# Kernel tuning notes

Measured on AMD Instinct MI355X. Metric: run time of the kernel, lower is better.

The kernel has to match this reference:

```python
import jax, jax.numpy as jnp
import numpy as np

N = 100000      # nodes
E = 1600000     # edges (before self loops)
F_IN = 128      # num_features
HEADS1, CH1 = 8, 8    # conv1: heads=8, out=8, concat -> 64
HEADS2, CH2 = 1, 16   # conv2: heads=1, out=16, concat=False
B = 64          # graphs in batch


def setup_inputs() -> dict:
    key = jax.random.key(0)
    ks = jax.random.split(key, 20)
    s = 0.05
    x = jax.random.normal(ks[0], (N, F_IN), dtype=jnp.float32)
    edge_index = jax.random.randint(ks[1], (2, E), 0, N, dtype=jnp.int64)
    batch = jnp.sort(jax.random.randint(ks[2], (N,), 0, B, dtype=jnp.int64))
    d = {
        'x': x, 'edge_index': edge_index, 'batch': batch,
        # conv1 params (GATv2: lin_l / lin_r with bias, att vector, output bias)
        'Wl1': jax.random.normal(ks[3], (F_IN, HEADS1 * CH1)) * s,
        'bl1': jnp.zeros((HEADS1 * CH1,), jnp.float32),
        'Wr1': jax.random.normal(ks[4], (F_IN, HEADS1 * CH1)) * s,
        'br1': jnp.zeros((HEADS1 * CH1,), jnp.float32),
        'att1': jax.random.normal(ks[5], (HEADS1, CH1)) * s,
        'bias1': jnp.zeros((HEADS1 * CH1,), jnp.float32),
        # conv2 params
        'Wl2': jax.random.normal(ks[6], (HEADS1 * CH1, HEADS2 * CH2)) * s,
        'bl2': jnp.zeros((HEADS2 * CH2,), jnp.float32),
        'Wr2': jax.random.normal(ks[7], (HEADS1 * CH1, HEADS2 * CH2)) * s,
        'br2': jnp.zeros((HEADS2 * CH2,), jnp.float32),
        'att2': jax.random.normal(ks[8], (HEADS2, CH2)) * s,
        'bias2': jnp.zeros((CH2,), jnp.float32),
        # classifier 16 -> 1
        'Wc': jax.random.normal(ks[9], (CH2, 1)) * s,
        'bc': jnp.zeros((1,), jnp.float32),
    }
    return d


def gatv2_layer(x, src, dst, Wl, bl, Wr, br, att, bias, heads, ch, concat):
    n = x.shape[0]
    xl = (x @ Wl + bl).reshape(n, heads, ch)   # source transform (messages)
    xr = (x @ Wr + br).reshape(n, heads, ch)   # target transform
    m = xl[src] + xr[dst]                      # [E, H, C]
    e = jax.nn.leaky_relu(m, 0.2)
    logits = jnp.einsum('ehc,hc->eh', e, att)  # [E, H]
    # segment softmax over incoming edges per target node
    mx = jax.ops.segment_max(logits, dst, num_segments=n)
    mx = jnp.where(jnp.isfinite(mx), mx, 0.0)
    ex = jnp.exp(logits - mx[dst])
    denom = jax.ops.segment_sum(ex, dst, num_segments=n)
    alpha = ex / (denom[dst] + 1e-16)
    out = jax.ops.segment_sum(alpha[:, :, None] * xl[src], dst, num_segments=n)
    out = out.reshape(n, heads * ch) if concat else out.mean(axis=1)
    return out + bias


def reference(x, edge_index, batch, Wl1, bl1, Wr1, br1, att1, bias1,
              Wl2, bl2, Wr2, br2, att2, bias2, Wc, bc):
    n = x.shape[0]
    loops = jnp.arange(n, dtype=edge_index.dtype)
    src = jnp.concatenate([edge_index[0], loops])   # add self loops (PyG default)
    dst = jnp.concatenate([edge_index[1], loops])

    h = gatv2_layer(x, src, dst, Wl1, bl1, Wr1, br1, att1, bias1, HEADS1, CH1, True)
    h = jax.nn.elu(h)
    h = gatv2_layer(h, src, dst, Wl2, bl2, Wr2, br2, att2, bias2, HEADS2, CH2, False)

    counts = jax.ops.segment_sum(jnp.ones((n,), h.dtype), batch, num_segments=B)
    pooled = jax.ops.segment_sum(h, batch, num_segments=B) / jnp.clip(counts, 1.0)[:, None]
    out = (pooled @ Wc + bc).reshape(-1)            # [B]
    return out, pooled
```

## Files before the change

kernel.cpp:

```cpp
#include <hip/hip_runtime.h>
#include <cstdint>
#include <cstddef>

#define F_IN   128
#define HC1    64
#define CH2_   16
#define NB     64
#define BUKPAD 8192

typedef __attribute__((ext_vector_type(8))) short bf16x8;
typedef __attribute__((ext_vector_type(4))) float f32x4;

__global__ void fill_f32(float* __restrict__ p, float v, int n) {
  int i = blockIdx.x * blockDim.x + threadIdx.x;
  int stride = gridDim.x * blockDim.x;
  for (; i < n; i += stride) p[i] = v;
}

__device__ __forceinline__ unsigned short f2bf_rne(float v) {
  unsigned int u = __float_as_uint(v);
  unsigned int r = (u + 0x7FFFu + ((u >> 16) & 1u)) >> 16;
  return (unsigned short)r;
}
__device__ __forceinline__ float bf2f(unsigned short b) {
  return __uint_as_float((unsigned int)b << 16);
}

template<int CTRL>
__device__ __forceinline__ float dpp_add(float v) {
  int j = __builtin_amdgcn_update_dpp(0, __float_as_int(v), CTRL, 0xF, 0xF, true);
  return v + __int_as_float(j);
}
__device__ __forceinline__ float sum16_dpp(float v) {
  v = dpp_add<0xB1>(v);
  v = dpp_add<0x4E>(v);
  v = dpp_add<0x141>(v);
  v = dpp_add<0x140>(v);
  return v;
}

__global__ void build_wfrag(const float* __restrict__ Wl, const float* __restrict__ Wr,
                            unsigned short* __restrict__ wfrag) {
  int idx = blockIdx.x * 256 + threadIdx.x;
  if (idx >= 16384) return;
  int e    = idx & 7;
  int lane = (idx >> 3) & 63;
  int tile = (idx >> 9) & 7;
  int ks   = idx >> 12;
  int k    = ks * 32 + (lane >> 4) * 8 + e;
  int col  = tile * 16 + (lane & 15);
  float v = (col < 64) ? Wl[k * 64 + col] : Wr[k * 64 + (col - 64)];
  wfrag[idx] = f2bf_rne(v);
}


__device__ void scatter_body(char* smem, const int* __restrict__ ei, int E, int E2,
                             int* __restrict__ gcnt, int* __restrict__ gbuk, int blk) {
  int* hbase = (int*)smem;
  int* hcnt  = hbase + 512;
  const int t = threadIdx.x;
  for (int i = t; i < 512; i += 256) { hbase[i] = 0; hcnt[i] = 0; }
  __syncthreads();
  int srcs[32], dsts[32];
  const int tile0 = blk * 8192;
#pragma unroll
  for (int k = 0; k < 32; ++k) {
    int e = tile0 + k * 256 + t;
    int s = -1, d = 0;
    if (e < E2) {
      if (e < E) { s = ei[e]; d = ei[E + e]; } else { s = d = e - E; }
      atomicAdd(&hbase[d >> 8], 1);
    }
    srcs[k] = s; dsts[k] = d;
  }
  __syncthreads();
  for (int i = t; i < 512; i += 256) {
    int c = hbase[i];
    hbase[i] = (c > 0) ? atomicAdd(&gcnt[i], c) : 0;
  }
  __syncthreads();
#pragma unroll
  for (int k = 0; k < 32; ++k) {
    if (srcs[k] >= 0) {
      int d = dsts[k], b = d >> 8;
      int r = atomicAdd(&hcnt[b], 1);
      int pl = hbase[b] + r;
      if (pl < BUKPAD) gbuk[(size_t)b * BUKPAD + pl] = (srcs[k] << 8) | (d & 255);
    }
  }
}

__device__ void gemm_body(char* smem, const float* __restrict__ x,
                          const unsigned short* __restrict__ wfrag,
                          const float* __restrict__ bl, const float* __restrict__ br,
                          unsigned short* __restrict__ ya, float* __restrict__ yb,
                          int n, int blk) {
  constexpr int RP = 136;
  unsigned short* axhi = (unsigned short*)smem;
  unsigned short* axlo = (unsigned short*)(smem + 17408);
  unsigned short* wf   = (unsigned short*)(smem + 34816);
  float* outs = (float*)smem;

  const int t = threadIdx.x;
  const int node0 = blk * 64;

  for (int i = t; i < 2048; i += 256)
    reinterpret_cast<int4*>(wf)[i] = reinterpret_cast<const int4*>(wfrag)[i];
  for (int i = t; i < 64 * 32; i += 256) {
    int row = i >> 5, kk = (i & 31) * 4;
    int node = node0 + row;
    float4 v = make_float4(0.f, 0.f, 0.f, 0.f);
    if (node < n) v = *reinterpret_cast<const float4*>(x + (size_t)node * 128 + kk);
    ushort4 hi, lo;
    hi.x = f2bf_rne(v.x); lo.x = f2bf_rne(v.x - bf2f(hi.x));
    hi.y = f2bf_rne(v.y); lo.y = f2bf_rne(v.y - bf2f(hi.y));
    hi.z = f2bf_rne(v.z); lo.z = f2bf_rne(v.z - bf2f(hi.z));
    hi.w = f2bf_rne(v.w); lo.w = f2bf_rne(v.w - bf2f(hi.w));
    *reinterpret_cast<ushort4*>(axhi + row * RP + kk) = hi;
    *reinterpret_cast<ushort4*>(axlo + row * RP + kk) = lo;
  }
  __syncthreads();

  const int wv   = t >> 6;
  const int lane = t & 63;
  const int mrow = lane & 15;
  const int kg   = lane >> 4;
  f32x4 acc[8];
#pragma unroll
  for (int i = 0; i < 8; ++i) acc[i] = (f32x4){0.f, 0.f, 0.f, 0.f};
  const int abase = (wv * 16 + mrow) * RP;
#pragma unroll
  for (int ks = 0; ks < 4; ++ks) {
    int aoff = abase + ks * 32 + kg * 8;
    bf16x8 ahi = *reinterpret_cast<const bf16x8*>(axhi + aoff);
    bf16x8 alo = *reinterpret_cast<const bf16x8*>(axlo + aoff);
#pragma unroll
    for (int tl = 0; tl < 8; ++tl) {
      bf16x8 b = *reinterpret_cast<const bf16x8*>(wf + ((ks * 8 + tl) * 64 + lane) * 8);
      acc[tl] = __builtin_amdgcn_mfma_f32_16x16x32_bf16(alo, b, acc[tl], 0, 0, 0);
      acc[tl] = __builtin_amdgcn_mfma_f32_16x16x32_bf16(ahi, b, acc[tl], 0, 0, 0);
    }
  }
  __syncthreads();
#pragma unroll
  for (int tl = 0; tl < 8; ++tl)
#pragma unroll
    for (int r = 0; r < 4; ++r) {
      int row = wv * 16 + kg * 4 + r;
      outs[row * 128 + tl * 16 + mrow] = acc[tl][r];
    }
  __syncthreads();
  for (int i = t; i < 64 * 64; i += 256) {
    int row = i >> 6, col = i & 63;
    int node = node0 + row;
    if (node < n) ya[(size_t)node * 64 + col] = f2bf_rne(outs[row * 128 + col] + bl[col]);
  }
  for (int i = t; i < 64 * 64; i += 256) {
    int row = i >> 6, col = i & 63;
    int node = node0 + row;
    if (node < n) yb[(size_t)node * 64 + col] = outs[row * 128 + 64 + col] + br[col];
  }
}

__global__ __launch_bounds__(256) void mega_scatter_gemm(
    const int* __restrict__ ei, int E, int E2,
    int* __restrict__ gcnt, int* __restrict__ gbuk, int nscat,
    const float* __restrict__ x, const unsigned short* __restrict__ wfrag,
    const float* __restrict__ bl, const float* __restrict__ br,
    unsigned short* __restrict__ ya, float* __restrict__ yb, int n) {
  __shared__ __align__(16) char smem[34816 + 32768];
  if ((int)blockIdx.x < nscat)
    scatter_body(smem, ei, E, E2, gcnt, gbuk, blockIdx.x);
  else
    gemm_body(smem, x, wfrag, bl, br, ya, yb, n, blockIdx.x - nscat);
}


__global__ void bucket_prefix(const int* __restrict__ gcnt, int nbuk,
                              int* __restrict__ gbase, int* __restrict__ row_start, int n) {
  int lane = threadIdx.x;
  int carry = 0;
  for (int basei = 0; basei < nbuk; basei += 64) {
    int i = basei + lane;
    int orig = (i < nbuk) ? gcnt[i] : 0;
    int v = orig;
    for (int off = 1; off < 64; off <<= 1) {
      int u = __shfl_up(v, off);
      if (lane >= off) v += u;
    }
    if (i < nbuk) gbase[i] = carry + v - orig;
    carry += __shfl(v, 63);
  }
  if (lane == 0) row_start[n] = carry;
}

__global__ void bucket_csr(const int* __restrict__ gcnt, const int* __restrict__ gbase,
                           const int* __restrict__ gbuk,
                           int* __restrict__ row_start, int* __restrict__ csr_src, int n) {
  const int b = blockIdx.x;
  const int t = threadIdx.x;
  const int node0 = b << 8;
  const int cntb = min(gcnt[b], BUKPAD);
  const int base = gbase[b];
  const int* buk = gbuk + (size_t)b * BUKPAD;
  __shared__ int h[256];
  __shared__ int off[256];
  h[t] = 0;
  __syncthreads();
  for (int i = t; i < cntb; i += 256) atomicAdd(&h[buk[i] & 255], 1);
  __syncthreads();
  off[t] = h[t];
  __syncthreads();
  for (int o = 1; o < 256; o <<= 1) {
    int u = (t >= o) ? off[t - o] : 0;
    __syncthreads();
    off[t] += u;
    __syncthreads();
  }
  int excl = off[t] - h[t];
  if (node0 + t < n) row_start[node0 + t] = base + excl;
  h[t] = excl;
  __syncthreads();
  for (int i = t; i < cntb; i += 256) {
    int p = buk[i];
    int r = atomicAdd(&h[p & 255], 1);
    csr_src[base + r] = p >> 8;
  }
}

__global__ void fused_layer1(const int* __restrict__ row_start, const int* __restrict__ csr_src,
                             const unsigned short* __restrict__ xl, const float* __restrict__ xr,
                             const float* __restrict__ att, const float* __restrict__ bias,
                             const float* __restrict__ Wl2, const float* __restrict__ bl2,
                             const float* __restrict__ Wr2, const float* __restrict__ br2,
                             unsigned short* __restrict__ xl2, float* __restrict__ xr2, int n) {
  __shared__ float Ws2[64 * 32];
  __shared__ float b2s[32];
  const int t = threadIdx.x;
  for (int i = t; i < 64 * 16; i += 256) {
    int l = i >> 4, j = i & 15;
    Ws2[l * 32 + j]      = Wl2[i];
    Ws2[l * 32 + 16 + j] = Wr2[i];
  }
  if (t < 16) { b2s[t] = bl2[t]; b2s[16 + t] = br2[t]; }
  __syncthreads();

  const int node = blockIdx.x * 4 + (t >> 6);
  if (node >= n) return;
  const int lane = t & 63;
  const int g = lane >> 4;
  const int q = lane & 15;
  const float4 attv = *reinterpret_cast<const float4*>(att + q * 4);
  const float4 xrv  = *reinterpret_cast<const float4*>(xr + (size_t)node * 64 + q * 4);
  const unsigned short* xlq = xl + q * 4;
  const int beg = row_start[node];
  const int total = row_start[node + 1] - beg;
  const float NEGB = -3.0e38f;
  float den = 0.0f;
  float4 acc = make_float4(0.f, 0.f, 0.f, 0.f);

  for (int base = 0; base < total; base += 64) {
    int idx = base + lane;
    int sidx = csr_src[beg + (idx < total ? idx : total - 1)];
    const int lim = min(64, total - base);
    for (int c0 = 0; c0 < lim; c0 += 16) {
      int ii[4]; int sv[4]; ushort4 u[4];
#pragma unroll
      for (int j = 0; j < 4; ++j) ii[j] = c0 + j * 4 + g;
#pragma unroll
      for (int j = 0; j < 4; ++j) sv[j] = __shfl(sidx, ii[j]);
#pragma unroll
      for (int j = 0; j < 4; ++j)
        u[j] = *reinterpret_cast<const ushort4*>(xlq + (size_t)sv[j] * 64);
#pragma unroll
      for (int j = 0; j < 4; ++j) {
        float x0 = bf2f(u[j].x), x1 = bf2f(u[j].y), x2 = bf2f(u[j].z), x3 = bf2f(u[j].w);
        float a0 = x0 + xrv.x; a0 = fmaxf(a0, 0.2f * a0);
        float a1 = x1 + xrv.y; a1 = fmaxf(a1, 0.2f * a1);
        float a2 = x2 + xrv.z; a2 = fmaxf(a2, 0.2f * a2);
        float a3 = x3 + xrv.w; a3 = fmaxf(a3, 0.2f * a3);
        float p = a0 * attv.x + a1 * attv.y + a2 * attv.z + a3 * attv.w;
        float v = dpp_add<0xB1>(p);
        float ex = __expf(ii[j] < lim ? v : NEGB);
        den  += ex;
        acc.x += ex * x0; acc.y += ex * x1;
        acc.z += ex * x2; acc.w += ex * x3;
      }
    }
  }
  acc.x += __shfl_xor(acc.x, 16); acc.y += __shfl_xor(acc.y, 16);
  acc.z += __shfl_xor(acc.z, 16); acc.w += __shfl_xor(acc.w, 16);
  acc.x += __shfl_xor(acc.x, 32); acc.y += __shfl_xor(acc.y, 32);
  acc.z += __shfl_xor(acc.z, 32); acc.w += __shfl_xor(acc.w, 32);
  den += __shfl_xor(den, 16);
  den += __shfl_xor(den, 32);
  const float inv = 1.0f / (den + 1e-16f);
  const float4 bi = *reinterpret_cast<const float4*>(bias + q * 4);
  float o0 = acc.x * inv + bi.x; o0 = o0 > 0.f ? o0 : __expf(o0) - 1.0f;
  float o1 = acc.y * inv + bi.y; o1 = o1 > 0.f ? o1 : __expf(o1) - 1.0f;
  float o2 = acc.z * inv + bi.z; o2 = o2 > 0.f ? o2 : __expf(o2) - 1.0f;
  float o3 = acc.w * inv + bi.w; o3 = o3 > 0.f ? o3 : __expf(o3) - 1.0f;

  int srcl = lane >> 2;
  float c0v = __shfl(o0, srcl);
  float c1v = __shfl(o1, srcl);
  float c2v = __shfl(o2, srcl);
  float c3v = __shfl(o3, srcl);
  int r = lane & 3;
  float o = (r == 0) ? c0v : (r == 1) ? c1v : (r == 2) ? c2v : c3v;

  const int j    = lane & 31;
  const int half = lane >> 5;
  float part2 = 0.0f;
#pragma unroll 8
  for (int l = 0; l < 32; ++l) {
    int src = half * 32 + l;
    float ov = __shfl(o, src);
    part2 += ov * Ws2[src * 32 + j];
  }
  part2 += __shfl_xor(part2, 32);
  if (lane < 16)      xl2[(size_t)node * 16 + j]        = f2bf_rne(part2 + b2s[j]);
  else if (lane < 32) xr2[(size_t)node * 16 + (j - 16)] = part2 + b2s[j];
}

__global__ void fused_layer2(const int* __restrict__ row_start, const int* __restrict__ csr_src,
                             const unsigned short* __restrict__ xl, const float* __restrict__ xr,
                             const float* __restrict__ att, const float* __restrict__ bias,
                             float* __restrict__ out, int n) {
  int node = blockIdx.x * 16 + (threadIdx.x >> 4);
  if (node >= n) return;
  const int lane = threadIdx.x & 63;
  const int c = lane & 15;
  const int gbase = lane & 48;
  const float attv = att[c];
  const float xrv  = xr[(size_t)node * 16 + c];
  const int beg = row_start[node];
  const int total = row_start[node + 1] - beg;
  const float NEGB = -3.0e38f;
  float den = 0.0f, acc = 0.0f;

  for (int base = 0; base < total; base += 16) {
    int wi = base + c;
    int sidx = csr_src[beg + (wi < total ? wi : total - 1)];
    const int lim = min(16, total - base);
    for (int c0 = 0; c0 < lim; c0 += 4) {
      int sv[4]; float xv[4];
#pragma unroll
      for (int j = 0; j < 4; ++j) sv[j] = __shfl(sidx, gbase + c0 + j);
#pragma unroll
      for (int j = 0; j < 4; ++j)
        xv[j] = bf2f(xl[(size_t)sv[j] * 16 + c]);
#pragma unroll
      for (int j = 0; j < 4; ++j) {
        float a = xv[j] + xrv; a = fmaxf(a, 0.2f * a);
        float v = sum16_dpp(a * attv);
        float ex = __expf((c0 + j) < lim ? v : NEGB);
        den += ex;
        acc += ex * xv[j];
      }
    }
  }
  out[(size_t)node * 16 + c] = acc / (den + 1e-16f) + bias[c];
}


__global__ void pool_kernel(const float* __restrict__ h2, const int* __restrict__ batch,
                            float* __restrict__ sums, float* __restrict__ cnts, int n) {
  __shared__ float ls[NB * CH2_];
  __shared__ float lc[NB];
  for (int i = threadIdx.x; i < NB * CH2_; i += blockDim.x) ls[i] = 0.0f;
  for (int i = threadIdx.x; i < NB; i += blockDim.x) lc[i] = 0.0f;
  __syncthreads();
  int total = n * 16;
  int stride = gridDim.x * blockDim.x;
  for (int i = blockIdx.x * blockDim.x + threadIdx.x; i < total; i += stride) {
    int node = i >> 4, c = i & 15;
    int b = batch[node];
    atomicAdd(&ls[b * 16 + c], h2[i]);
    if (c == 0) atomicAdd(&lc[b], 1.0f);
  }
  __syncthreads();
  for (int i = threadIdx.x; i < NB * CH2_; i += blockDim.x)
    if (ls[i] != 0.0f) atomicAdd(&sums[i], ls[i]);
  for (int i = threadIdx.x; i < NB; i += blockDim.x)
    if (lc[i] != 0.0f) atomicAdd(&cnts[i], lc[i]);
}

__global__ void classifier(const float* __restrict__ sums, const float* __restrict__ cnts,
                           const float* __restrict__ Wc, const float* __restrict__ bc,
                           float* __restrict__ out) {
  int b = threadIdx.x;
  if (b >= NB) return;
  float cnt = cnts[b];
  cnt = cnt > 1.0f ? cnt : 1.0f;
  float acc = 0.0f;
  for (int c = 0; c < 16; ++c) {
    float p = sums[b * 16 + c] / cnt;
    out[NB + b * 16 + c] = p;
    acc += p * Wc[c];
  }
  out[b] = acc + bc[0];
}

extern "C" void kernel_launch(void* const* d_in, const int* in_sizes, int n_in,
                              void* d_out, int out_size, void* d_ws, size_t ws_size,
                              hipStream_t stream) {
  const float* x     = (const float*)d_in[0];
  const int*   ei    = (const int*)d_in[1];
  const int*   batch = (const int*)d_in[2];
  const float* Wl1   = (const float*)d_in[3];
  const float* bl1   = (const float*)d_in[4];
  const float* Wr1   = (const float*)d_in[5];
  const float* br1   = (const float*)d_in[6];
  const float* att1  = (const float*)d_in[7];
  const float* bias1 = (const float*)d_in[8];
  const float* Wl2   = (const float*)d_in[9];
  const float* bl2   = (const float*)d_in[10];
  const float* Wr2   = (const float*)d_in[11];
  const float* br2   = (const float*)d_in[12];
  const float* att2  = (const float*)d_in[13];
  const float* bias2 = (const float*)d_in[14];
  const float* Wc    = (const float*)d_in[15];
  const float* bc    = (const float*)d_in[16];
  float* out = (float*)d_out;

  const int N  = in_sizes[0] / F_IN;
  const int E  = in_sizes[1] / 2;
  const int E2 = E + N;
  const int nbuk = (N + 255) >> 8;
  const int nscat = (E2 + 8191) / 8192;
  const int ngemm = (N + 63) / 64;

  float* ws   = (float*)d_ws;
  unsigned short* xl1 = (unsigned short*)ws;
  float* xr1  = (float*)(xl1 + (size_t)N * 64);
  unsigned short* xl2 = (unsigned short*)(xr1 + (size_t)N * 64);
  float* xr2  = (float*)(xl2 + (size_t)N * 16);
  float* h2   = xr2 + (size_t)N * 16;
  int* irow   = (int*)(h2 + (size_t)N * 16);
  int* icsr   = irow + (N + 1);
  int* gcnt   = icsr + E2;
  int* gbase  = gcnt + 512;
  int* gbuk   = gbase + 513 + 2;
  unsigned short* wfrag =
      (unsigned short*)(((uintptr_t)(gbuk + (size_t)nbuk * BUKPAD) + 15) & ~(uintptr_t)15);
  float* sums = (float*)(wfrag + 16384);
  float* cnts = sums + NB * CH2_;

  fill_f32<<<1, 256, 0, stream>>>((float*)gcnt, 0.0f, 512);
  build_wfrag<<<64, 256, 0, stream>>>(Wl1, Wr1, wfrag);

  mega_scatter_gemm<<<nscat + ngemm, 256, 0, stream>>>(
      ei, E, E2, gcnt, gbuk, nscat, x, wfrag, bl1, br1, xl1, xr1, N);

  bucket_prefix<<<1, 64, 0, stream>>>(gcnt, nbuk, gbase, irow, N);
  bucket_csr<<<nbuk, 256, 0, stream>>>(gcnt, gbase, gbuk, irow, icsr, N);

  fused_layer1<<<(N + 3) / 4, 256, 0, stream>>>(
      irow, icsr, xl1, xr1, att1, bias1, Wl2, bl2, Wr2, br2, xl2, xr2, N);

  fused_layer2<<<(N + 15) / 16, 256, 0, stream>>>(irow, icsr, xl2, xr2, att2, bias2, h2, N);

  fill_f32<<<1, 256, 0, stream>>>(sums, 0.0f, NB * CH2_ + NB);
  pool_kernel<<<256, 256, 0, stream>>>(h2, batch, sums, cnts, N);
  classifier<<<1, 64, 0, stream>>>(sums, cnts, Wc, bc, out);
}
```

Baseline: 213.7 us.

## Fuse layer2 with pooling, fold prefix scan and fills into neighbors

Cuts four kernel launches. The zero-fills move into build_wfrag. The bucket prefix scan is recomputed per block inside bucket_csr with a shared-memory reduction over the preceding bucket counts. Layer-2 aggregation is fused with graph pooling, so h2 is no longer written to or read back from global memory. In exchange, each fused block does shared-memory atomics and a flush of its 1024-entry partial sums to global atomics (about 6250 blocks instead of 256). Each CSR block also redundantly sums up to ~390 counts.

```diff
diff --git a/kernel.cpp b/kernel.cpp
--- a/kernel.cpp
+++ b/kernel.cpp
@@ -10,12 +10,6 @@
 
 typedef __attribute__((ext_vector_type(8))) short bf16x8;
 typedef __attribute__((ext_vector_type(4))) float f32x4;
-
-__global__ void fill_f32(float* __restrict__ p, float v, int n) {
-  int i = blockIdx.x * blockDim.x + threadIdx.x;
-  int stride = gridDim.x * blockDim.x;
-  for (; i < n; i += stride) p[i] = v;
-}
 
 __device__ __forceinline__ unsigned short f2bf_rne(float v) {
   unsigned int u = __float_as_uint(v);
@@ -40,8 +34,14 @@
 }
 
 __global__ void build_wfrag(const float* __restrict__ Wl, const float* __restrict__ Wr,
-                            unsigned short* __restrict__ wfrag) {
-  int idx = blockIdx.x * 256 + threadIdx.x;
+                            unsigned short* __restrict__ wfrag,
+                            int* __restrict__ gcnt, float* __restrict__ sums) {
+  const int t = threadIdx.x;
+  if (blockIdx.x == 0) { gcnt[t] = 0; gcnt[256 + t] = 0; }
+  if (blockIdx.x == 1) {
+    for (int i = t; i < NB * CH2_ + NB; i += 256) sums[i] = 0.0f;
+  }
+  int idx = blockIdx.x * 256 + t;
   if (idx >= 16384) return;
   int e    = idx & 7;
   int lane = (idx >> 3) & 63;
@@ -175,33 +175,24 @@
     gemm_body(smem, x, wfrag, bl, br, ya, yb, n, blockIdx.x - nscat);
 }
 
-
-__global__ void bucket_prefix(const int* __restrict__ gcnt, int nbuk,
-                              int* __restrict__ gbase, int* __restrict__ row_start, int n) {
-  int lane = threadIdx.x;
-  int carry = 0;
-  for (int basei = 0; basei < nbuk; basei += 64) {
-    int i = basei + lane;
-    int orig = (i < nbuk) ? gcnt[i] : 0;
-    int v = orig;
-    for (int off = 1; off < 64; off <<= 1) {
-      int u = __shfl_up(v, off);
-      if (lane >= off) v += u;
-    }
-    if (i < nbuk) gbase[i] = carry + v - orig;
-    carry += __shfl(v, 63);
-  }
-  if (lane == 0) row_start[n] = carry;
-}
-
-__global__ void bucket_csr(const int* __restrict__ gcnt, const int* __restrict__ gbase,
-                           const int* __restrict__ gbuk,
-                           int* __restrict__ row_start, int* __restrict__ csr_src, int n) {
+__global__ void bucket_csr(const int* __restrict__ gcnt, const int* __restrict__ gbuk,
+                           int* __restrict__ row_start, int* __restrict__ csr_src,
+                           int n, int nbuk) {
   const int b = blockIdx.x;
   const int t = threadIdx.x;
+  __shared__ int red[256];
+  int s = 0;
+  for (int i = t; i < b; i += 256) s += gcnt[i];
+  red[t] = s;
+  __syncthreads();
+  for (int o = 128; o > 0; o >>= 1) {
+    if (t < o) red[t] += red[t + o];
+    __syncthreads();
+  }
+  const int base = red[0];
+
   const int node0 = b << 8;
   const int cntb = min(gcnt[b], BUKPAD);
-  const int base = gbase[b];
   const int* buk = gbuk + (size_t)b * BUKPAD;
   __shared__ int h[256];
   __shared__ int off[256];
@@ -219,6 +210,7 @@
   }
   int excl = off[t] - h[t];
   if (node0 + t < n) row_start[node0 + t] = base + excl;
+  if (b == nbuk - 1 && t == 0) row_start[n] = base + cntb;
   h[t] = excl;
   __syncthreads();
   for (int i = t; i < cntb; i += 256) {
@@ -323,66 +315,60 @@
   else if (lane < 32) xr2[(size_t)node * 16 + (j - 16)] = part2 + b2s[j];
 }
 
-__global__ void fused_layer2(const int* __restrict__ row_start, const int* __restrict__ csr_src,
-                             const unsigned short* __restrict__ xl, const float* __restrict__ xr,
-                             const float* __restrict__ att, const float* __restrict__ bias,
-                             float* __restrict__ out, int n) {
-  int node = blockIdx.x * 16 + (threadIdx.x >> 4);
-  if (node >= n) return;
-  const int lane = threadIdx.x & 63;
-  const int c = lane & 15;
-  const int gbase = lane & 48;
-  const float attv = att[c];
-  const float xrv  = xr[(size_t)node * 16 + c];
-  const int beg = row_start[node];
-  const int total = row_start[node + 1] - beg;
-  const float NEGB = -3.0e38f;
-  float den = 0.0f, acc = 0.0f;
-
-  for (int base = 0; base < total; base += 16) {
-    int wi = base + c;
-    int sidx = csr_src[beg + (wi < total ? wi : total - 1)];
-    const int lim = min(16, total - base);
-    for (int c0 = 0; c0 < lim; c0 += 4) {
-      int sv[4]; float xv[4];
-#pragma unroll
-      for (int j = 0; j < 4; ++j) sv[j] = __shfl(sidx, gbase + c0 + j);
-#pragma unroll
-      for (int j = 0; j < 4; ++j)
-        xv[j] = bf2f(xl[(size_t)sv[j] * 16 + c]);
-#pragma unroll
-      for (int j = 0; j < 4; ++j) {
-        float a = xv[j] + xrv; a = fmaxf(a, 0.2f * a);
-        float v = sum16_dpp(a * attv);
-        float ex = __expf((c0 + j) < lim ? v : NEGB);
-        den += ex;
-        acc += ex * xv[j];
-      }
-    }
-  }
-  out[(size_t)node * 16 + c] = acc / (den + 1e-16f) + bias[c];
-}
-
-
-__global__ void pool_kernel(const float* __restrict__ h2, const int* __restrict__ batch,
-                            float* __restrict__ sums, float* __restrict__ cnts, int n) {
+__global__ void fused_layer2_pool(const int* __restrict__ row_start, const int* __restrict__ csr_src,
+                                  const unsigned short* __restrict__ xl, const float* __restrict__ xr,
+                                  const float* __restrict__ att, const float* __restrict__ bias,
+                                  const int* __restrict__ batch,
+                                  float* __restrict__ sums, float* __restrict__ cnts, int n) {
   __shared__ float ls[NB * CH2_];
   __shared__ float lc[NB];
-  for (int i = threadIdx.x; i < NB * CH2_; i += blockDim.x) ls[i] = 0.0f;
-  for (int i = threadIdx.x; i < NB; i += blockDim.x) lc[i] = 0.0f;
-  __syncthreads();
-  int total = n * 16;
-  int stride = gridDim.x * blockDim.x;
-  for (int i = blockIdx.x * blockDim.x + threadIdx.x; i < total; i += stride) {
-    int node = i >> 4, c = i & 15;
+  const int t = threadIdx.x;
+  for (int i = t; i < NB * CH2_; i += 256) ls[i] = 0.0f;
+  for (int i = t; i < NB; i += 256) lc[i] = 0.0f;
+  __syncthreads();
+
+  const int node = blockIdx.x * 16 + (t >> 4);
+  const int lane = t & 63;
+  const int c = lane & 15;
+  if (node < n) {
+    const int gbase = lane & 48;
+    const float attv = att[c];
+    const float xrv  = xr[(size_t)node * 16 + c];
+    const int beg = row_start[node];
+    const int total = row_start[node + 1] - beg;
+    const float NEGB = -3.0e38f;
+    float den = 0.0f, acc = 0.0f;
+
+    for (int base = 0; base < total; base += 16) {
+      int wi = base + c;
+      int sidx = csr_src[beg + (wi < total ? wi : total - 1)];
+      const int lim = min(16, total - base);
+      for (int c0 = 0; c0 < lim; c0 += 4) {
+        int sv[4]; float xv[4];
+#pragma unroll
+        for (int j = 0; j < 4; ++j) sv[j] = __shfl(sidx, gbase + c0 + j);
+#pragma unroll
+        for (int j = 0; j < 4; ++j)
+          xv[j] = bf2f(xl[(size_t)sv[j] * 16 + c]);
+#pragma unroll
+        for (int j = 0; j < 4; ++j) {
+          float a = xv[j] + xrv; a = fmaxf(a, 0.2f * a);
+          float v = sum16_dpp(a * attv);
+          float ex = __expf((c0 + j) < lim ? v : NEGB);
+          den += ex;
+          acc += ex * xv[j];
+        }
+      }
+    }
+    float val = acc / (den + 1e-16f) + bias[c];
     int b = batch[node];
-    atomicAdd(&ls[b * 16 + c], h2[i]);
+    atomicAdd(&ls[b * 16 + c], val);
     if (c == 0) atomicAdd(&lc[b], 1.0f);
   }
   __syncthreads();
-  for (int i = threadIdx.x; i < NB * CH2_; i += blockDim.x)
+  for (int i = t; i < NB * CH2_; i += 256)
     if (ls[i] != 0.0f) atomicAdd(&sums[i], ls[i]);
-  for (int i = threadIdx.x; i < NB; i += blockDim.x)
+  for (int i = t; i < NB; i += 256)
     if (lc[i] != 0.0f) atomicAdd(&cnts[i], lc[i]);
 }
 
@@ -436,32 +422,27 @@
   float* xr1  = (float*)(xl1 + (size_t)N * 64);
   unsigned short* xl2 = (unsigned short*)(xr1 + (size_t)N * 64);
   float* xr2  = (float*)(xl2 + (size_t)N * 16);
-  float* h2   = xr2 + (size_t)N * 16;
-  int* irow   = (int*)(h2 + (size_t)N * 16);
+  int* irow   = (int*)(xr2 + (size_t)N * 16);
   int* icsr   = irow + (N + 1);
   int* gcnt   = icsr + E2;
-  int* gbase  = gcnt + 512;
-  int* gbuk   = gbase + 513 + 2;
+  int* gbuk   = gcnt + 512 + 4;
   unsigned short* wfrag =
       (unsigned short*)(((uintptr_t)(gbuk + (size_t)nbuk * BUKPAD) + 15) & ~(uintptr_t)15);
   float* sums = (float*)(wfrag + 16384);
   float* cnts = sums + NB * CH2_;
 
-  fill_f32<<<1, 256, 0, stream>>>((float*)gcnt, 0.0f, 512);
-  build_wfrag<<<64, 256, 0, stream>>>(Wl1, Wr1, wfrag);
+  build_wfrag<<<64, 256, 0, stream>>>(Wl1, Wr1, wfrag, gcnt, sums);
 
   mega_scatter_gemm<<<nscat + ngemm, 256, 0, stream>>>(
       ei, E, E2, gcnt, gbuk, nscat, x, wfrag, bl1, br1, xl1, xr1, N);
 
-  bucket_prefix<<<1, 64, 0, stream>>>(gcnt, nbuk, gbase, irow, N);
-  bucket_csr<<<nbuk, 256, 0, stream>>>(gcnt, gbase, gbuk, irow, icsr, N);
+  bucket_csr<<<nbuk, 256, 0, stream>>>(gcnt, gbuk, irow, icsr, N, nbuk);
 
   fused_layer1<<<(N + 3) / 4, 256, 0, stream>>>(
       irow, icsr, xl1, xr1, att1, bias1, Wl2, bl2, Wr2, br2, xl2, xr2, N);
 
-  fused_layer2<<<(N + 15) / 16, 256, 0, stream>>>(irow, icsr, xl2, xr2, att2, bias2, h2, N);
-
-  fill_f32<<<1, 256, 0, stream>>>(sums, 0.0f, NB * CH2_ + NB);
-  pool_kernel<<<256, 256, 0, stream>>>(h2, batch, sums, cnts, N);
+  fused_layer2_pool<<<(N + 15) / 16, 256, 0, stream>>>(
+      irow, icsr, xl2, xr2, att2, bias2, batch, sums, cnts, N);
+
   classifier<<<1, 64, 0, stream>>>(sums, cnts, Wc, bc, out);
 }
```

Result: slower. 220.6 us (+3.2%).
